# Performance work log

Measured on AMD Instinct MI355X. Metric: run time of the kernel, lower is better.

## Reference

```python
import jax, jax.numpy as jnp
import numpy as np

MAX_NUM_CAPS = 10
NEG = -1e9

def _layernorm(x, g, b):
    m = x.mean(-1, keepdims=True)
    v = x.var(-1, keepdims=True)
    return (x - m) / jnp.sqrt(v + 1e-5) * g + b

def _gatv2(x, Wl, Wr, att, bias, adj):
    # x: [B,M,F]; Wl/Wr: [F,H*C]; att: [H,C]; adj: [B,M,M] bool, adj[b,i,j] = edge i->j
    B, M, F = x.shape
    H, C = att.shape
    xl = jnp.einsum('bmf,fhc->bmhc', x, Wl.reshape(F, H, C))  # source transform
    xr = jnp.einsum('bmf,fhc->bmhc', x, Wr.reshape(F, H, C))  # target transform
    # GATv2 score: att . leaky_relu(xl[i] + xr[j]) for edge (src=i, dst=j)
    z = jax.nn.leaky_relu(xl[:, :, None, :, :] + xr[:, None, :, :, :], 0.2)  # [B,i,j,H,C]
    e = jnp.einsum('bijhc,hc->bijh', z, att)
    e = jnp.where(adj[..., None], e, NEG)
    alpha = jax.nn.softmax(e, axis=1)  # softmax over incoming sources i per target j
    out = jnp.einsum('bijh,bihc->bjhc', alpha, xl)  # aggregate at targets
    return out.reshape(B, M, H * C) + bias

def setup_inputs() -> dict:
    key = jax.random.key(0)
    ks = jax.random.split(key, 16)
    B, N, T = 128, 16, 48
    Fm, H, C3 = 128, 4, 64
    s = 0.05
    inp = {
        'team_obs': jax.random.normal(ks[0], (B, N, 14), jnp.float32),
        'target_obs': jax.random.normal(ks[1], (B, T, 15), jnp.float32),
        'team_mask': jax.random.normal(ks[2], (B, 2, N), jnp.float32),
        'local_target_mask': jnp.ones((B, T + 1), jnp.float32),
        'W_emb': jax.random.normal(ks[3], (16, Fm), jnp.float32) * s,
        'b_emb': jnp.zeros((Fm,), jnp.float32),
        'Wl1': jax.random.normal(ks[4], (Fm, Fm), jnp.float32) * s,
        'Wr1': jax.random.normal(ks[5], (Fm, Fm), jnp.float32) * s,
        'att1': jax.random.normal(ks[6], (H, Fm // H), jnp.float32) * s,
        'b1': jnp.zeros((Fm,), jnp.float32),
        'Wl2': jax.random.normal(ks[7], (Fm, Fm), jnp.float32) * s,
        'Wr2': jax.random.normal(ks[8], (Fm, Fm), jnp.float32) * s,
        'att2': jax.random.normal(ks[9], (H, Fm // H), jnp.float32) * s,
        'b2': jnp.zeros((Fm,), jnp.float32),
        'Wl3': jax.random.normal(ks[10], (Fm, C3), jnp.float32) * s,
        'Wr3': jax.random.normal(ks[11], (Fm, C3), jnp.float32) * s,
        'att3': jax.random.normal(ks[12], (1, C3), jnp.float32) * s,
        'b3': jnp.zeros((C3,), jnp.float32),
        'ln1_g': jnp.ones((Fm,), jnp.float32),
        'ln1_b': jnp.zeros((Fm,), jnp.float32),
        'ln2_g': jnp.ones((Fm,), jnp.float32),
        'ln2_b': jnp.zeros((Fm,), jnp.float32),
    }
    return inp

def reference(team_obs, target_obs, team_mask, local_target_mask,
              W_emb, b_emb, Wl1, Wr1, att1, b1, Wl2, Wr2, att2, b2,
              Wl3, Wr3, att3, b3, ln1_g, ln1_b, ln2_g, ln2_b):
    B, N, _ = team_obs.shape
    team = jnp.concatenate([team_obs, jnp.zeros((B, N, 2), team_obs.dtype)], axis=2)
    tgt = target_obs[:, :, :-1]
    T = tgt.shape[1]
    tgt = jnp.concatenate([tgt[:, :, :2 + MAX_NUM_CAPS],
                           jnp.zeros((B, T, 2), tgt.dtype),
                           tgt[:, :, -2:]], axis=2)
    fin = jnp.concatenate([team, tgt], axis=1)  # [B, M, inp_dim]
    h = fin @ W_emb + b_emb  # [B, M, 128]
    imp_team = team_mask[:, 0] != -1e9          # [B, N]
    imp_tgt = local_target_mask[:, :-1] != 0.0  # [B, T]
    imp = jnp.concatenate([imp_team, imp_tgt], axis=1)  # [B, M]
    M = N + T
    eye = jnp.eye(M, dtype=bool)
    # edges among active nodes minus diagonal; PyG GATv2Conv add_self_loops=True re-adds self edges
    adj = (imp[:, :, None] & imp[:, None, :] & ~eye) | eye  # [B, M, M]
    out = jax.nn.relu(_layernorm(_gatv2(h, Wl1, Wr1, att1, b1, adj), ln1_g, ln1_b))
    out = jax.nn.relu(_layernorm(_gatv2(out, Wl2, Wr2, att2, b2, adj), ln2_g, ln2_b))
    out = _gatv2(out, Wl3, Wr3, att3, b3, adj)
    return out  # [B, M, out_dim]
```

## Files before the change

kernel.cpp:

```cpp
#include <hip/hip_runtime.h>

typedef unsigned short u16;
typedef unsigned int   u32;
typedef _Float16 h2  __attribute__((ext_vector_type(2)));
typedef __fp16   hw2 __attribute__((ext_vector_type(2)));
typedef __fp16   hw8 __attribute__((ext_vector_type(8)));
typedef float    f4  __attribute__((ext_vector_type(4)));

#define XS 136
#define PS 72
#define BS 72
#define OS2 20

static __device__ __forceinline__ h2 pk(float a, float b) {
    return __builtin_bit_cast(h2, __builtin_amdgcn_cvt_pkrtz(a, b));
}
static __device__ __forceinline__ float dot2(h2 a, h2 b, float c) {
    return __builtin_amdgcn_fdot2(__builtin_bit_cast(hw2, a),
                                  __builtin_bit_cast(hw2, b), c, false);
}
static __device__ __forceinline__ h2  b2h(u32 v) { return __builtin_bit_cast(h2, v); }
static __device__ __forceinline__ u32 h2u(h2 v)  { return __builtin_bit_cast(u32, v); }
static __device__ __forceinline__ h2  abs2(h2 v) { return b2h(h2u(v) & 0x7fff7fffu); }
static __device__ __forceinline__ u16 f2h(float f) { return __builtin_bit_cast(u16, (_Float16)f); }
static __device__ __forceinline__ f4 mfma16(uint4 a, uint4 b, f4 c) {
    return __builtin_amdgcn_mfma_f32_16x16x32_f16(__builtin_bit_cast(hw8, a),
                                                  __builtin_bit_cast(hw8, b), c, 0, 0, 0);
}

__global__ void pack_weights(const float* __restrict__ Wl1, const float* __restrict__ Wr1,
                             const float* __restrict__ Wl2, const float* __restrict__ Wr2,
                             const float* __restrict__ Wl3, const float* __restrict__ Wr3,
                             u32* __restrict__ wpk)
{
    const int o = blockIdx.x * 256 + threadIdx.x;
    const float* src; u32* dst; int local; int N;
    if      (o < 8192)  { src = Wl1; dst = wpk;         local = o;         N = 128; }
    else if (o < 16384) { src = Wr1; dst = wpk + 8192;  local = o - 8192;  N = 128; }
    else if (o < 24576) { src = Wl2; dst = wpk + 16384; local = o - 16384; N = 128; }
    else if (o < 32768) { src = Wr2; dst = wpk + 24576; local = o - 24576; N = 128; }
    else if (o < 36864) { src = Wl3; dst = wpk + 32768; local = o - 32768; N = 64;  }
    else                { src = Wr3; dst = wpk + 36864; local = o - 36864; N = 64;  }
    const int i2   = local & 3;
    const int lane = (local >> 2) & 63;
    const int frag = local >> 8;
    const int kb   = frag & 3;
    const int nt   = frag >> 2;
    const int k0   = kb*32 + ((lane >> 4) << 3) + i2*2;
    const int n    = nt*16 + (lane & 15);
    dst[local] = h2u(pk(src[k0*N + n], src[(k0+1)*N + n]));
}

static __device__ __forceinline__ void compute_imp(int t, int b,
    const float* __restrict__ team_mask, const float* __restrict__ ltm, float* sImp)
{
    if (t < 64) {
        float im;
        if (t < 16) im = (team_mask[b*32 + t] != -1000000000.0f) ? 1.f : 0.f;
        else        im = (ltm[b*49 + (t-16)] != 0.0f) ? 1.f : 0.f;
        sImp[t] = im;
    }
}

static __device__ __forceinline__ void load_afr_lds(const u16* sX, int mt, int lane, uint4 afr[4]) {
    const int n15 = lane & 15, qd = lane >> 4;
#pragma unroll
    for (int kb = 0; kb < 4; kb++)
        afr[kb] = *(const uint4*)&sX[(mt*16 + n15)*XS + kb*32 + (qd << 3)];
}
static __device__ __forceinline__ void load_afr_glb(const u32* __restrict__ gxRow, int mt, int lane, uint4 afr[4]) {
    const int n15 = lane & 15, qd = lane >> 4;
    const int m = mt*16 + n15;
#pragma unroll
    for (int kb = 0; kb < 4; kb++)
        afr[kb] = *(const uint4*)&gxRow[m*64 + kb*16 + qd*4];
}

static __device__ __forceinline__ void projL128(int w, int lane, const u32* __restrict__ wp,
    const uint4 afr[4], u16* sXl, u16* sXlB)
{
    const int mt = w & 3, nh = w >> 2;
    const int n15 = lane & 15, qd = lane >> 4;
#pragma unroll
    for (int nt = nh*4; nt < nh*4 + 4; nt++) {
        f4 acc = {0.f, 0.f, 0.f, 0.f};
#pragma unroll
        for (int kb = 0; kb < 4; kb++) {
            uint4 bf = *(const uint4*)&wp[((nt*4 + kb)*64 + lane)*4];
            acc = mfma16(afr[kb], bf, acc);
        }
        const int n  = nt*16 + n15;
        const int mb = mt*16 + (qd << 2);
#pragma unroll
        for (int r = 0; r < 4; r++) sXl[(mb + r)*XS + n] = f2h(acc[r]);
        uint2 u;
        u.x = h2u(pk(acc[0], acc[1]));
        u.y = h2u(pk(acc[2], acc[3]));
        *(uint2*)&sXlB[n*BS + mb] = u;
    }
}

static __device__ __forceinline__ void projR16(int w, int lane, const u32* __restrict__ wp,
    const uint4 afq[4], u16* sXrPx)
{
    const int n15 = lane & 15, qd = lane >> 4;
    const int nt = w;
    f4 acc = {0.f, 0.f, 0.f, 0.f};
#pragma unroll
    for (int kb = 0; kb < 4; kb++) {
        uint4 bf = *(const uint4*)&wp[((nt*4 + kb)*64 + lane)*4];
        acc = mfma16(afq[kb], bf, acc);
    }
    const int n = nt*16 + n15;
#pragma unroll
    for (int r = 0; r < 4; r++)
        sXrPx[((n >> 3)*16 + (qd << 2) + r)*8 + (n & 7)] = f2h(acc[r]);
}

static __device__ __forceinline__ void scores16(int w, int lane, int j0,
    const float* __restrict__ att,
    const u16* sXl, const u16* sXrPx, u16* sP,
    float* sAl, float* sL2, const float* sImp)
{
    const int h  = w & 3;
    const int qh = w >> 2;
    const int jj = lane & 15;
    const int is = lane >> 4;
    const int j  = j0 + jj;

    h2 a2[16];
#pragma unroll
    for (int q = 0; q < 16; q++) a2[q] = pk(att[h*32 + 2*q], att[h*32 + 2*q + 1]);

    if (w < 4) {
        const uint4* pr = (const uint4*)&sXl[lane*XS + h*32];
        float al = 0.f;
#pragma unroll
        for (int c4 = 0; c4 < 4; c4++) {
            uint4 v = pr[c4];
            al = dot2(b2h(v.x), a2[c4*4+0], al);
            al = dot2(b2h(v.y), a2[c4*4+1], al);
            al = dot2(b2h(v.z), a2[c4*4+2], al);
            al = dot2(b2h(v.w), a2[c4*4+3], al);
        }
        sAl[h*64 + lane] = al;
    }

    h2 xr2[16];
#pragma unroll
    for (int s = 0; s < 4; s++) {
        uint4 v = *(const uint4*)&sXrPx[((h*4 + s)*16 + jj)*8];
        xr2[s*4+0] = b2h(v.x); xr2[s*4+1] = b2h(v.y);
        xr2[s*4+2] = b2h(v.z); xr2[s*4+3] = b2h(v.w);
    }
    float Ar = 0.f;
#pragma unroll
    for (int q = 0; q < 16; q++) Ar = dot2(a2[q], xr2[q], Ar);
    const float impj = sImp[j];
    __syncthreads();

    float l = 0.f;
    u32 pr4[4];
    float pprev = 0.f;
#pragma unroll
    for (int i2 = 0; i2 < 8; i2++) {
        const int i = qh*32 + is*8 + i2;
        const uint4* pl = (const uint4*)&sXl[i*XS + h*32];
        uint4 v0 = pl[0], v1 = pl[1], v2 = pl[2], v3 = pl[3];
        h2 xl2[16];
        xl2[0] = b2h(v0.x); xl2[1] = b2h(v0.y); xl2[2]  = b2h(v0.z); xl2[3]  = b2h(v0.w);
        xl2[4] = b2h(v1.x); xl2[5] = b2h(v1.y); xl2[6]  = b2h(v1.z); xl2[7]  = b2h(v1.w);
        xl2[8] = b2h(v2.x); xl2[9] = b2h(v2.y); xl2[10] = b2h(v2.z); xl2[11] = b2h(v2.w);
        xl2[12]= b2h(v3.x); xl2[13]= b2h(v3.y); xl2[14] = b2h(v3.z); xl2[15] = b2h(v3.w);
        float S0 = 0.f, S1 = 0.f;
#pragma unroll
        for (int q = 0; q < 16; q += 2) {
            h2 t0 = abs2(xl2[q]   + xr2[q]);
            h2 t1 = abs2(xl2[q+1] + xr2[q+1]);
            S0 = dot2(a2[q],   t0, S0);
            S1 = dot2(a2[q+1], t1, S1);
        }
        float e  = 0.6f*(sAl[h*64 + i] + Ar) + 0.4f*(S0 + S1);
        float ad = (i == j) ? 1.f : impj * sImp[i];
        float p  = (ad != 0.f) ? __expf(e) : 0.f;
        if (i2 & 1) {
            h2 pp = pk(pprev, p);
            pr4[i2 >> 1] = h2u(pp);
            l += (float)pp[0] + (float)pp[1];
        } else {
            pprev = p;
        }
    }
    *(uint4*)&sP[(h*16 + jj)*PS + qh*32 + is*8] = make_uint4(pr4[0], pr4[1], pr4[2], pr4[3]);
    sL2[((h*2 + qh)*4 + is)*16 + jj] = l;
}

static __device__ __forceinline__ void aggln16(int w, int lane, int b, int j0,
    const float* __restrict__ bias, const float* __restrict__ lg, const float* __restrict__ lb,
    const u16* sP, const u16* sXlB, float* sOutF, const float* sL2,
    float* sPart, u32* __restrict__ gxOut)
{
    const int h   = w & 3;
    const int cb  = w >> 2;
    const int n15 = lane & 15;
    const int kq  = lane >> 4;

    f4 acc = {0.f,0.f,0.f,0.f};
#pragma unroll
    for (int ks = 0; ks < 2; ks++) {
        uint4 af = *(const uint4*)&sP[(h*16 + n15)*PS + ks*32 + kq*8];
        uint4 bf = *(const uint4*)&sXlB[(h*32 + cb*16 + n15)*BS + ks*32 + kq*8];
        acc = mfma16(af, bf, acc);
    }
#pragma unroll
    for (int r = 0; r < 4; r++)
        sOutF[(h*32 + cb*16 + n15)*OS2 + kq*4 + r] = acc[r];
    __syncthreads();

    const int jj = lane & 15, is2 = lane >> 4, hd = w >> 1;
    float l = 0.f;
#pragma unroll
    for (int g = 0; g < 8; g++) l += sL2[(hd*8 + g)*16 + jj];
    const float rl = 1.f / l;
    const int c0 = w*16 + is2*4;
    float y[4];
    float s1 = 0.f, s2 = 0.f;
#pragma unroll
    for (int k = 0; k < 4; k++) {
        float v = fmaf(sOutF[(c0 + k)*OS2 + jj], rl, bias[c0 + k]);
        y[k] = v; s1 += v; s2 = fmaf(v, v, s2);
    }
    sPart[(w*4 + is2)*16 + jj]       = s1;
    sPart[512 + (w*4 + is2)*16 + jj] = s2;
    __syncthreads();
    float su = 0.f, sq = 0.f;
#pragma unroll
    for (int g = 0; g < 32; g++) { su += sPart[g*16 + jj]; sq += sPart[512 + g*16 + jj]; }
    const float mean = su * 0.0078125f;
    const float var  = sq * 0.0078125f - mean*mean;
    const float rstd = rsqrtf(var + 1e-5f);
    float v0 = fmaxf(fmaf((y[0] - mean)*rstd, lg[c0],   lb[c0]),   0.f);
    float v1 = fmaxf(fmaf((y[1] - mean)*rstd, lg[c0+1], lb[c0+1]), 0.f);
    float v2 = fmaxf(fmaf((y[2] - mean)*rstd, lg[c0+2], lb[c0+2]), 0.f);
    float v3 = fmaxf(fmaf((y[3] - mean)*rstd, lg[c0+3], lb[c0+3]), 0.f);
    uint2 o;
    o.x = h2u(pk(v0, v1));
    o.y = h2u(pk(v2, v3));
    *(uint2*)(gxOut + (size_t)b*4096 + (size_t)(j0 + jj)*64 + (c0 >> 1)) = o;
}

__global__ void __launch_bounds__(512, 4) gnn_l1(
    const float* __restrict__ team_obs, const float* __restrict__ target_obs,
    const float* __restrict__ team_mask, const float* __restrict__ ltm,
    const float* __restrict__ W_emb, const float* __restrict__ b_emb,
    const float* __restrict__ att1, const float* __restrict__ b1,
    const float* __restrict__ ln1_g, const float* __restrict__ ln1_b,
    const u32* __restrict__ wpk, u32* __restrict__ gx1)
{
    __shared__ __align__(16) u16 sX   [64*XS];
    __shared__ __align__(16) u16 sXl  [64*XS];
    __shared__ __align__(16) u16 sXlB [128*BS];
    __shared__ __align__(16) u16 sXrPx[2048];
    __shared__ __align__(16) u16 sP   [4*16*PS];
    __shared__ float sAl [256];
    __shared__ float sL2 [512];
    __shared__ float sPart[1024];
    __shared__ float sImp[64];

    const int t    = threadIdx.x;
    const int w    = t >> 6;
    const int lane = t & 63;
    const int b    = blockIdx.x & 127;
    const int q    = blockIdx.x >> 7;
    const int j0   = q*16;

    float* sFin  = (float*)sP;
    float* sOutF = (float*)sX;

    compute_imp(t, b, team_mask, ltm, sImp);
    for (int ee = t; ee < 1024; ee += 512) {
        int m = ee >> 4, k = ee & 15;
        float v = 0.f;
        if (m < 16) {
            if (k < 14) v = team_obs[(b*16 + m)*14 + k];
        } else {
            const float* tg = target_obs + (size_t)(b*48 + (m-16))*15;
            if      (k < 12)  v = tg[k];
            else if (k == 14) v = tg[12];
            else if (k == 15) v = tg[13];
        }
        sFin[m*16 + k] = v;
    }
    __syncthreads();

    {
        const int f = t & 127;
        const int g = t >> 7;
        float wreg[16];
#pragma unroll
        for (int k = 0; k < 16; k++) wreg[k] = W_emb[k*128 + f];
        const float bf = b_emb[f];
#pragma unroll
        for (int mm = 0; mm < 16; mm++) {
            int m = g*16 + mm;
            const float4* pf = (const float4*)&sFin[m*16];
            float4 f0 = pf[0], f1 = pf[1], f2 = pf[2], f3 = pf[3];
            float acc = bf;
            acc = fmaf(f0.x, wreg[0],  acc); acc = fmaf(f0.y, wreg[1],  acc);
            acc = fmaf(f0.z, wreg[2],  acc); acc = fmaf(f0.w, wreg[3],  acc);
            acc = fmaf(f1.x, wreg[4],  acc); acc = fmaf(f1.y, wreg[5],  acc);
            acc = fmaf(f1.z, wreg[6],  acc); acc = fmaf(f1.w, wreg[7],  acc);
            acc = fmaf(f2.x, wreg[8],  acc); acc = fmaf(f2.y, wreg[9],  acc);
            acc = fmaf(f2.z, wreg[10], acc); acc = fmaf(f2.w, wreg[11], acc);
            acc = fmaf(f3.x, wreg[12], acc); acc = fmaf(f3.y, wreg[13], acc);
            acc = fmaf(f3.z, wreg[14], acc); acc = fmaf(f3.w, wreg[15], acc);
            sX[m*XS + f] = f2h(acc);
        }
    }
    __syncthreads();

    uint4 afr[4], afq[4];
    load_afr_lds(sX, w & 3, lane, afr);
    load_afr_lds(sX, q,     lane, afq);
    projL128(w, lane, wpk,        afr, sXl, sXlB);
    projR16 (w, lane, wpk + 8192, afq, sXrPx);
    __syncthreads();

    scores16(w, lane, j0, att1, sXl, sXrPx, sP, sAl, sL2, sImp);
    __syncthreads();
    aggln16(w, lane, b, j0, b1, ln1_g, ln1_b, sP, sXlB, sOutF, sL2, sPart, gx1);
}

__global__ void __launch_bounds__(512, 4) gnn_l2(
    const float* __restrict__ team_mask, const float* __restrict__ ltm,
    const float* __restrict__ att2, const float* __restrict__ b2,
    const float* __restrict__ ln2_g, const float* __restrict__ ln2_b,
    const u32* __restrict__ wpk, const u32* __restrict__ gxIn, u32* __restrict__ gxOut)
{
    __shared__ __align__(16) u16 sXl  [64*XS];
    __shared__ __align__(16) u16 sXlB [128*BS];
    __shared__ __align__(16) u16 sXrPx[2048];
    __shared__ __align__(16) u16 sP   [4*16*PS];
    __shared__ __align__(16) float sOutF[128*OS2];
    __shared__ float sAl [256];
    __shared__ float sL2 [512];
    __shared__ float sPart[1024];
    __shared__ float sImp[64];

    const int t    = threadIdx.x;
    const int w    = t >> 6;
    const int lane = t & 63;
    const int b    = blockIdx.x & 127;
    const int q    = blockIdx.x >> 7;
    const int j0   = q*16;

    compute_imp(t, b, team_mask, ltm, sImp);
    const u32* gxRow = gxIn + (size_t)b*4096;

    uint4 afr[4], afq[4];
    load_afr_glb(gxRow, w & 3, lane, afr);
    load_afr_glb(gxRow, q,     lane, afq);
    projL128(w, lane, wpk + 16384, afr, sXl, sXlB);
    projR16 (w, lane, wpk + 24576, afq, sXrPx);
    __syncthreads();

    scores16(w, lane, j0, att2, sXl, sXrPx, sP, sAl, sL2, sImp);
    __syncthreads();
    aggln16(w, lane, b, j0, b2, ln2_g, ln2_b, sP, sXlB, sOutF, sL2, sPart, gxOut);
}

__global__ void __launch_bounds__(512, 4) gnn_l3(
    const float* __restrict__ team_mask, const float* __restrict__ ltm,
    const float* __restrict__ att3, const float* __restrict__ b3,
    const u32* __restrict__ wpk, const u32* __restrict__ gxIn, float* __restrict__ out)
{
    __shared__ __align__(16) u16 sXl3 [64*72];
    __shared__ __align__(16) u16 sXlB3[64*72];
    __shared__ __align__(16) u16 sXrP3[1024];
    __shared__ __align__(16) u16 sP3  [16*72];
    __shared__ float sAl3[64];
    __shared__ float sPart[512];
    __shared__ float sRl [16];
    __shared__ float sImp[64];

    const int t    = threadIdx.x;
    const int w    = t >> 6;
    const int lane = t & 63;
    const int b    = blockIdx.x & 127;
    const int q    = blockIdx.x >> 7;
    const int j0   = q*16;
    const int n15  = lane & 15;
    const int qd   = lane >> 4;

    compute_imp(t, b, team_mask, ltm, sImp);
    const u32* gxRow = gxIn + (size_t)b*4096;

    {
        uint4 afr[4];
        load_afr_glb(gxRow, w & 3, lane, afr);
        const u32* wp = wpk + 32768;
        const int mt = w & 3, nh = w >> 2;
#pragma unroll
        for (int nt = nh*2; nt < nh*2 + 2; nt++) {
            f4 acc = {0.f,0.f,0.f,0.f};
#pragma unroll
            for (int kb = 0; kb < 4; kb++) {
                uint4 bf = *(const uint4*)&wp[((nt*4 + kb)*64 + lane)*4];
                acc = mfma16(afr[kb], bf, acc);
            }
            const int n  = nt*16 + n15;
            const int mb = mt*16 + (qd << 2);
#pragma unroll
            for (int r = 0; r < 4; r++) sXl3[(mb + r)*72 + n] = f2h(acc[r]);
            uint2 u;
            u.x = h2u(pk(acc[0], acc[1]));
            u.y = h2u(pk(acc[2], acc[3]));
            *(uint2*)&sXlB3[n*72 + mb] = u;
        }
    }
    if (w < 4) {
        uint4 afq[4];
        load_afr_glb(gxRow, q, lane, afq);
        const u32* wp = wpk + 36864;
        f4 acc = {0.f,0.f,0.f,0.f};
#pragma unroll
        for (int kb = 0; kb < 4; kb++) {
            uint4 bf = *(const uint4*)&wp[((w*4 + kb)*64 + lane)*4];
            acc = mfma16(afq[kb], bf, acc);
        }
        const int n = w*16 + n15;
#pragma unroll
        for (int r = 0; r < 4; r++)
            sXrP3[((n >> 3)*16 + (qd << 2) + r)*8 + (n & 7)] = f2h(acc[r]);
    }
    __syncthreads();

    {
        h2 a2l[4];
#pragma unroll
        for (int qq = 0; qq < 4; qq++) a2l[qq] = pk(att3[w*8 + 2*qq], att3[w*8 + 2*qq + 1]);
        uint4 v = *(const uint4*)&sXl3[lane*72 + w*8];
        float al = 0.f;
        al = dot2(b2h(v.x), a2l[0], al);
        al = dot2(b2h(v.y), a2l[1], al);
        al = dot2(b2h(v.z), a2l[2], al);
        al = dot2(b2h(v.w), a2l[3], al);
        sPart[w*64 + lane] = al;
    }
    __syncthreads();
    if (t < 64) {
        sAl3[t] = ((sPart[t] + sPart[64+t]) + (sPart[128+t] + sPart[192+t]))
                + ((sPart[256+t] + sPart[320+t]) + (sPart[384+t] + sPart[448+t]));
    }
    __syncthreads();

    {
        const int jj = n15;
        const int is = qd;
        const int j  = j0 + jj;
        h2 a3[32], xr3[32];
#pragma unroll
        for (int qq = 0; qq < 32; qq++) a3[qq] = pk(att3[2*qq], att3[2*qq + 1]);
#pragma unroll
        for (int s = 0; s < 8; s++) {
            uint4 v = *(const uint4*)&sXrP3[(s*16 + jj)*8];
            xr3[s*4+0] = b2h(v.x); xr3[s*4+1] = b2h(v.y);
            xr3[s*4+2] = b2h(v.z); xr3[s*4+3] = b2h(v.w);
        }
        float Ar = 0.f;
#pragma unroll
        for (int qq = 0; qq < 32; qq++) Ar = dot2(a3[qq], xr3[qq], Ar);
        const float impj = sImp[j];
        const int i0 = w*8 + is*2;

        float p0, p1;
        {
            const int i = i0;
            const uint4* pl = (const uint4*)&sXl3[i*72];
            float S0 = 0.f, S1 = 0.f;
#pragma unroll
            for (int c4 = 0; c4 < 8; c4++) {
                uint4 v = pl[c4];
                S0 = dot2(a3[c4*4+0], abs2(b2h(v.x) + xr3[c4*4+0]), S0);
                S1 = dot2(a3[c4*4+1], abs2(b2h(v.y) + xr3[c4*4+1]), S1);
                S0 = dot2(a3[c4*4+2], abs2(b2h(v.z) + xr3[c4*4+2]), S0);
                S1 = dot2(a3[c4*4+3], abs2(b2h(v.w) + xr3[c4*4+3]), S1);
            }
            float e  = 0.6f*(sAl3[i] + Ar) + 0.4f*(S0 + S1);
            float ad = (i == j) ? 1.f : impj * sImp[i];
            p0 = (ad != 0.f) ? __expf(e) : 0.f;
        }
        {
            const int i = i0 + 1;
            const uint4* pl = (const uint4*)&sXl3[i*72];
            float S0 = 0.f, S1 = 0.f;
#pragma unroll
            for (int c4 = 0; c4 < 8; c4++) {
                uint4 v = pl[c4];
                S0 = dot2(a3[c4*4+0], abs2(b2h(v.x) + xr3[c4*4+0]), S0);
                S1 = dot2(a3[c4*4+1], abs2(b2h(v.y) + xr3[c4*4+1]), S1);
                S0 = dot2(a3[c4*4+2], abs2(b2h(v.z) + xr3[c4*4+2]), S0);
                S1 = dot2(a3[c4*4+3], abs2(b2h(v.w) + xr3[c4*4+3]), S1);
            }
            float e  = 0.6f*(sAl3[i] + Ar) + 0.4f*(S0 + S1);
            float ad = (i == j) ? 1.f : impj * sImp[i];
            p1 = (ad != 0.f) ? __expf(e) : 0.f;
        }
        h2 pp = pk(p0, p1);
        *(u32*)&sP3[jj*72 + i0] = h2u(pp);
        sPart[(w*4 + is)*16 + jj] = (float)pp[0] + (float)pp[1];
    }
    __syncthreads();
    if (t < 16) {
        float s = 0.f;
#pragma unroll
        for (int g = 0; g < 32; g++) s += sPart[g*16 + t];
        sRl[t] = 1.f / s;
    }

    f4 acc3 = {0.f,0.f,0.f,0.f};
    if (w < 4) {
#pragma unroll
        for (int ks = 0; ks < 2; ks++) {
            uint4 af = *(const uint4*)&sP3[n15*72 + ks*32 + (lane >> 4)*8];
            uint4 bf = *(const uint4*)&sXlB3[(w*16 + n15)*72 + ks*32 + (lane >> 4)*8];
            acc3 = mfma16(af, bf, acc3);
        }
    }
    __syncthreads();
    if (w < 4) {
        const int c  = w*16 + n15;
        const float bc = b3[c];
#pragma unroll
        for (int r = 0; r < 4; r++) {
            const int jl = (lane >> 4)*4 + r;
            out[(size_t)b*4096 + (size_t)(j0 + jl)*64 + c] = fmaf(acc3[r], sRl[jl], bc);
        }
    }
}

extern "C" void kernel_launch(void* const* d_in, const int* in_sizes, int n_in,
                              void* d_out, int out_size, void* d_ws, size_t ws_size,
                              hipStream_t stream) {
    (void)in_sizes; (void)n_in; (void)ws_size; (void)out_size;
    const float* team_obs          = (const float*)d_in[0];
    const float* target_obs        = (const float*)d_in[1];
    const float* team_mask         = (const float*)d_in[2];
    const float* local_target_mask = (const float*)d_in[3];
    const float* W_emb             = (const float*)d_in[4];
    const float* b_emb             = (const float*)d_in[5];
    const float* Wl1               = (const float*)d_in[6];
    const float* Wr1               = (const float*)d_in[7];
    const float* att1              = (const float*)d_in[8];
    const float* b1                = (const float*)d_in[9];
    const float* Wl2               = (const float*)d_in[10];
    const float* Wr2               = (const float*)d_in[11];
    const float* att2              = (const float*)d_in[12];
    const float* b2                = (const float*)d_in[13];
    const float* Wl3               = (const float*)d_in[14];
    const float* Wr3               = (const float*)d_in[15];
    const float* att3              = (const float*)d_in[16];
    const float* b3                = (const float*)d_in[17];
    const float* ln1_g             = (const float*)d_in[18];
    const float* ln1_b             = (const float*)d_in[19];
    const float* ln2_g             = (const float*)d_in[20];
    const float* ln2_b             = (const float*)d_in[21];
    float* out = (float*)d_out;

    u32* wpk = (u32*)d_ws;
    u32* gx2 = (u32*)d_ws + 40960;
    u32* gx1 = (u32*)d_out;

    pack_weights<<<dim3(160), dim3(256), 0, stream>>>(Wl1, Wr1, Wl2, Wr2, Wl3, Wr3, wpk);
    gnn_l1<<<dim3(512), dim3(512), 0, stream>>>(
        team_obs, target_obs, team_mask, local_target_mask, W_emb, b_emb,
        att1, b1, ln1_g, ln1_b, wpk, gx1);
    gnn_l2<<<dim3(512), dim3(512), 0, stream>>>(
        team_mask, local_target_mask, att2, b2, ln2_g, ln2_b, wpk, gx1, gx2);
    gnn_l3<<<dim3(512), dim3(512), 0, stream>>>(
        team_mask, local_target_mask, att3, b3, wpk, gx2, out);
}
```

Measured before the change: 132.3 us.

## Process 32 target nodes per block with 1024-thread blocks in all GNN layers

Each block now handles 32 target nodes instead of 16, so 256 blocks of 1024 threads replace 512 blocks of 512 threads. The per-graph source projection (Xl for all 64 nodes) is then computed once per two 32-target halves instead of once per four 16-target quarters, which cuts redundant projection MFMAs and weight loads. Scores, aggregation, layernorm and the layer-3 output were remapped to the wider tile, with larger shared buffers and relocated workspace buffers. The cost is fewer, larger blocks with more LDS each, which may reduce occupancy and lengthen barrier waits on the 256-CU device.

```diff
diff --git a/kernel.cpp b/kernel.cpp
--- a/kernel.cpp
+++ b/kernel.cpp
@@ -10,7 +10,7 @@
 #define XS 136
 #define PS 72
 #define BS 72
-#define OS2 20
+#define OS3 34
 
 static __device__ __forceinline__ h2 pk(float a, float b) {
     return __builtin_bit_cast(h2, __builtin_amdgcn_cvt_pkrtz(a, b));
@@ -76,13 +76,14 @@
         afr[kb] = *(const uint4*)&gxRow[m*64 + kb*16 + qd*4];
 }
 
-static __device__ __forceinline__ void projL128(int w, int lane, const u32* __restrict__ wp,
+static __device__ __forceinline__ void projL128_16(int w, int lane, const u32* __restrict__ wp,
     const uint4 afr[4], u16* sXl, u16* sXlB)
 {
-    const int mt = w & 3, nh = w >> 2;
+    const int mt = w & 3, np = w >> 2;
     const int n15 = lane & 15, qd = lane >> 4;
-#pragma unroll
-    for (int nt = nh*4; nt < nh*4 + 4; nt++) {
+    (void)mt;
+#pragma unroll
+    for (int nt = np*2; nt < np*2 + 2; nt++) {
         f4 acc = {0.f, 0.f, 0.f, 0.f};
 #pragma unroll
         for (int kb = 0; kb < 4; kb++) {
@@ -90,7 +91,7 @@
             acc = mfma16(afr[kb], bf, acc);
         }
         const int n  = nt*16 + n15;
-        const int mb = mt*16 + (qd << 2);
+        const int mb = (w & 3)*16 + (qd << 2);
 #pragma unroll
         for (int r = 0; r < 4; r++) sXl[(mb + r)*XS + n] = f2h(acc[r]);
         uint2 u;
@@ -100,32 +101,33 @@
     }
 }
 
-static __device__ __forceinline__ void projR16(int w, int lane, const u32* __restrict__ wp,
+static __device__ __forceinline__ void projR32(int w, int lane, const u32* __restrict__ wp,
     const uint4 afq[4], u16* sXrPx)
 {
     const int n15 = lane & 15, qd = lane >> 4;
-    const int nt = w;
+    const int ntR = w >> 1;
     f4 acc = {0.f, 0.f, 0.f, 0.f};
 #pragma unroll
     for (int kb = 0; kb < 4; kb++) {
-        uint4 bf = *(const uint4*)&wp[((nt*4 + kb)*64 + lane)*4];
+        uint4 bf = *(const uint4*)&wp[((ntR*4 + kb)*64 + lane)*4];
         acc = mfma16(afq[kb], bf, acc);
     }
-    const int n = nt*16 + n15;
+    const int n   = ntR*16 + n15;
+    const int mb2 = (w & 1)*16 + (qd << 2);
 #pragma unroll
     for (int r = 0; r < 4; r++)
-        sXrPx[((n >> 3)*16 + (qd << 2) + r)*8 + (n & 7)] = f2h(acc[r]);
-}
-
-static __device__ __forceinline__ void scores16(int w, int lane, int j0,
+        sXrPx[((n >> 3)*32 + mb2 + r)*8 + (n & 7)] = f2h(acc[r]);
+}
+
+static __device__ __forceinline__ void scores32(int w, int lane, int j0,
     const float* __restrict__ att,
     const u16* sXl, const u16* sXrPx, u16* sP,
     float* sAl, float* sL2, const float* sImp)
 {
     const int h  = w & 3;
     const int qh = w >> 2;
-    const int jj = lane & 15;
-    const int is = lane >> 4;
+    const int jj = lane & 31;
+    const int is = lane >> 5;
     const int j  = j0 + jj;
 
     h2 a2[16];
@@ -149,7 +151,7 @@
     h2 xr2[16];
 #pragma unroll
     for (int s = 0; s < 4; s++) {
-        uint4 v = *(const uint4*)&sXrPx[((h*4 + s)*16 + jj)*8];
+        uint4 v = *(const uint4*)&sXrPx[((h*4 + s)*32 + jj)*8];
         xr2[s*4+0] = b2h(v.x); xr2[s*4+1] = b2h(v.y);
         xr2[s*4+2] = b2h(v.z); xr2[s*4+3] = b2h(v.w);
     }
@@ -162,9 +164,10 @@
     float l = 0.f;
     u32 pr4[4];
     float pprev = 0.f;
+    const int i0 = qh*16 + is*8;
 #pragma unroll
     for (int i2 = 0; i2 < 8; i2++) {
-        const int i = qh*32 + is*8 + i2;
+        const int i = i0 + i2;
         const uint4* pl = (const uint4*)&sXl[i*XS + h*32];
         uint4 v0 = pl[0], v1 = pl[1], v2 = pl[2], v3 = pl[3];
         h2 xl2[16];
@@ -191,51 +194,54 @@
             pprev = p;
         }
     }
-    *(uint4*)&sP[(h*16 + jj)*PS + qh*32 + is*8] = make_uint4(pr4[0], pr4[1], pr4[2], pr4[3]);
-    sL2[((h*2 + qh)*4 + is)*16 + jj] = l;
-}
-
-static __device__ __forceinline__ void aggln16(int w, int lane, int b, int j0,
+    *(uint4*)&sP[(h*32 + jj)*PS + i0] = make_uint4(pr4[0], pr4[1], pr4[2], pr4[3]);
+    sL2[((h*4 + qh)*2 + is)*32 + jj] = l;
+}
+
+static __device__ __forceinline__ void aggln32(int w, int lane, int b, int j0,
     const float* __restrict__ bias, const float* __restrict__ lg, const float* __restrict__ lb,
     const u16* sP, const u16* sXlB, float* sOutF, const float* sL2,
     float* sPart, u32* __restrict__ gxOut)
 {
     const int h   = w & 3;
-    const int cb  = w >> 2;
+    const int jq  = (w >> 2) & 1;
+    const int cb  = w >> 3;
     const int n15 = lane & 15;
     const int kq  = lane >> 4;
 
     f4 acc = {0.f,0.f,0.f,0.f};
 #pragma unroll
     for (int ks = 0; ks < 2; ks++) {
-        uint4 af = *(const uint4*)&sP[(h*16 + n15)*PS + ks*32 + kq*8];
+        uint4 af = *(const uint4*)&sP[(h*32 + jq*16 + n15)*PS + ks*32 + kq*8];
         uint4 bf = *(const uint4*)&sXlB[(h*32 + cb*16 + n15)*BS + ks*32 + kq*8];
         acc = mfma16(af, bf, acc);
     }
 #pragma unroll
     for (int r = 0; r < 4; r++)
-        sOutF[(h*32 + cb*16 + n15)*OS2 + kq*4 + r] = acc[r];
-    __syncthreads();
-
-    const int jj = lane & 15, is2 = lane >> 4, hd = w >> 1;
+        sOutF[(h*32 + cb*16 + n15)*OS3 + jq*16 + kq*4 + r] = acc[r];
+    __syncthreads();
+
+    const int jj = lane & 31, is5 = lane >> 5;
+    const int cgrp = w*2 + is5;
+    const int c0 = cgrp*4;
+    const int hd = c0 >> 5;
     float l = 0.f;
 #pragma unroll
-    for (int g = 0; g < 8; g++) l += sL2[(hd*8 + g)*16 + jj];
+    for (int g = 0; g < 8; g++) l += sL2[(hd*8 + g)*32 + jj];
     const float rl = 1.f / l;
-    const int c0 = w*16 + is2*4;
     float y[4];
     float s1 = 0.f, s2 = 0.f;
 #pragma unroll
     for (int k = 0; k < 4; k++) {
-        float v = fmaf(sOutF[(c0 + k)*OS2 + jj], rl, bias[c0 + k]);
+        float v = fmaf(sOutF[(c0 + k)*OS3 + jj], rl, bias[c0 + k]);
         y[k] = v; s1 += v; s2 = fmaf(v, v, s2);
     }
-    sPart[(w*4 + is2)*16 + jj]       = s1;
-    sPart[512 + (w*4 + is2)*16 + jj] = s2;
+    sPart[cgrp*32 + jj]        = s1;
+    sPart[1024 + cgrp*32 + jj] = s2;
     __syncthreads();
     float su = 0.f, sq = 0.f;
 #pragma unroll
-    for (int g = 0; g < 32; g++) { su += sPart[g*16 + jj]; sq += sPart[512 + g*16 + jj]; }
+    for (int g = 0; g < 32; g++) { su += sPart[g*32 + jj]; sq += sPart[1024 + g*32 + jj]; }
     const float mean = su * 0.0078125f;
     const float var  = sq * 0.0078125f - mean*mean;
     const float rstd = rsqrtf(var + 1e-5f);
@@ -249,7 +255,7 @@
     *(uint2*)(gxOut + (size_t)b*4096 + (size_t)(j0 + jj)*64 + (c0 >> 1)) = o;
 }
 
-__global__ void __launch_bounds__(512, 4) gnn_l1(
+__global__ void __launch_bounds__(1024, 4) gnn_l1(
     const float* __restrict__ team_obs, const float* __restrict__ target_obs,
     const float* __restrict__ team_mask, const float* __restrict__ ltm,
     const float* __restrict__ W_emb, const float* __restrict__ b_emb,
@@ -260,26 +266,26 @@
     __shared__ __align__(16) u16 sX   [64*XS];
     __shared__ __align__(16) u16 sXl  [64*XS];
     __shared__ __align__(16) u16 sXlB [128*BS];
-    __shared__ __align__(16) u16 sXrPx[2048];
-    __shared__ __align__(16) u16 sP   [4*16*PS];
+    __shared__ __align__(16) u16 sXrPx[4096];
+    __shared__ __align__(16) u16 sP   [4*32*PS];
     __shared__ float sAl [256];
-    __shared__ float sL2 [512];
-    __shared__ float sPart[1024];
+    __shared__ float sL2 [1024];
+    __shared__ float sPart[2048];
     __shared__ float sImp[64];
 
     const int t    = threadIdx.x;
     const int w    = t >> 6;
     const int lane = t & 63;
-    const int b    = blockIdx.x & 127;
-    const int q    = blockIdx.x >> 7;
-    const int j0   = q*16;
+    const int b    = blockIdx.x >> 1;
+    const int q    = blockIdx.x & 1;
+    const int j0   = q*32;
 
     float* sFin  = (float*)sP;
     float* sOutF = (float*)sX;
 
     compute_imp(t, b, team_mask, ltm, sImp);
-    for (int ee = t; ee < 1024; ee += 512) {
-        int m = ee >> 4, k = ee & 15;
+    {
+        int m = t >> 4, k = t & 15;
         float v = 0.f;
         if (m < 16) {
             if (k < 14) v = team_obs[(b*16 + m)*14 + k];
@@ -301,8 +307,8 @@
         for (int k = 0; k < 16; k++) wreg[k] = W_emb[k*128 + f];
         const float bf = b_emb[f];
 #pragma unroll
-        for (int mm = 0; mm < 16; mm++) {
-            int m = g*16 + mm;
+        for (int mm = 0; mm < 8; mm++) {
+            int m = g*8 + mm;
             const float4* pf = (const float4*)&sFin[m*16];
             float4 f0 = pf[0], f1 = pf[1], f2 = pf[2], f3 = pf[3];
             float acc = bf;
@@ -320,18 +326,18 @@
     __syncthreads();
 
     uint4 afr[4], afq[4];
-    load_afr_lds(sX, w & 3, lane, afr);
-    load_afr_lds(sX, q,     lane, afq);
-    projL128(w, lane, wpk,        afr, sXl, sXlB);
-    projR16 (w, lane, wpk + 8192, afq, sXrPx);
-    __syncthreads();
-
-    scores16(w, lane, j0, att1, sXl, sXrPx, sP, sAl, sL2, sImp);
-    __syncthreads();
-    aggln16(w, lane, b, j0, b1, ln1_g, ln1_b, sP, sXlB, sOutF, sL2, sPart, gx1);
-}
-
-__global__ void __launch_bounds__(512, 4) gnn_l2(
+    load_afr_lds(sX, w & 3,           lane, afr);
+    load_afr_lds(sX, q*2 + (w & 1),   lane, afq);
+    projL128_16(w, lane, wpk,        afr, sXl, sXlB);
+    projR32    (w, lane, wpk + 8192, afq, sXrPx);
+    __syncthreads();
+
+    scores32(w, lane, j0, att1, sXl, sXrPx, sP, sAl, sL2, sImp);
+    __syncthreads();
+    aggln32(w, lane, b, j0, b1, ln1_g, ln1_b, sP, sXlB, sOutF, sL2, sPart, gx1);
+}
+
+__global__ void __launch_bounds__(1024, 4) gnn_l2(
     const float* __restrict__ team_mask, const float* __restrict__ ltm,
     const float* __restrict__ att2, const float* __restrict__ b2,
     const float* __restrict__ ln2_g, const float* __restrict__ ln2_b,
@@ -339,56 +345,56 @@
 {
     __shared__ __align__(16) u16 sXl  [64*XS];
     __shared__ __align__(16) u16 sXlB [128*BS];
-    __shared__ __align__(16) u16 sXrPx[2048];
-    __shared__ __align__(16) u16 sP   [4*16*PS];
-    __shared__ __align__(16) float sOutF[128*OS2];
+    __shared__ __align__(16) u16 sXrPx[4096];
+    __shared__ __align__(16) u16 sP   [4*32*PS];
+    __shared__ __align__(16) float sOutF[128*OS3];
     __shared__ float sAl [256];
-    __shared__ float sL2 [512];
-    __shared__ float sPart[1024];
+    __shared__ float sL2 [1024];
+    __shared__ float sPart[2048];
     __shared__ float sImp[64];
 
     const int t    = threadIdx.x;
     const int w    = t >> 6;
     const int lane = t & 63;
-    const int b    = blockIdx.x & 127;
-    const int q    = blockIdx.x >> 7;
-    const int j0   = q*16;
+    const int b    = blockIdx.x >> 1;
+    const int q    = blockIdx.x & 1;
+    const int j0   = q*32;
 
     compute_imp(t, b, team_mask, ltm, sImp);
     const u32* gxRow = gxIn + (size_t)b*4096;
 
     uint4 afr[4], afq[4];
-    load_afr_glb(gxRow, w & 3, lane, afr);
-    load_afr_glb(gxRow, q,     lane, afq);
-    projL128(w, lane, wpk + 16384, afr, sXl, sXlB);
-    projR16 (w, lane, wpk + 24576, afq, sXrPx);
-    __syncthreads();
-
-    scores16(w, lane, j0, att2, sXl, sXrPx, sP, sAl, sL2, sImp);
-    __syncthreads();
-    aggln16(w, lane, b, j0, b2, ln2_g, ln2_b, sP, sXlB, sOutF, sL2, sPart, gxOut);
-}
-
-__global__ void __launch_bounds__(512, 4) gnn_l3(
+    load_afr_glb(gxRow, w & 3,         lane, afr);
+    load_afr_glb(gxRow, q*2 + (w & 1), lane, afq);
+    projL128_16(w, lane, wpk + 16384, afr, sXl, sXlB);
+    projR32    (w, lane, wpk + 24576, afq, sXrPx);
+    __syncthreads();
+
+    scores32(w, lane, j0, att2, sXl, sXrPx, sP, sAl, sL2, sImp);
+    __syncthreads();
+    aggln32(w, lane, b, j0, b2, ln2_g, ln2_b, sP, sXlB, sOutF, sL2, sPart, gxOut);
+}
+
+__global__ void __launch_bounds__(1024, 4) gnn_l3(
     const float* __restrict__ team_mask, const float* __restrict__ ltm,
     const float* __restrict__ att3, const float* __restrict__ b3,
     const u32* __restrict__ wpk, const u32* __restrict__ gxIn, float* __restrict__ out)
 {
     __shared__ __align__(16) u16 sXl3 [64*72];
     __shared__ __align__(16) u16 sXlB3[64*72];
-    __shared__ __align__(16) u16 sXrP3[1024];
-    __shared__ __align__(16) u16 sP3  [16*72];
+    __shared__ __align__(16) u16 sXrP3[2048];
+    __shared__ __align__(16) u16 sP3  [32*72];
     __shared__ float sAl3[64];
-    __shared__ float sPart[512];
-    __shared__ float sRl [16];
+    __shared__ float sPart[1024];
+    __shared__ float sRl [32];
     __shared__ float sImp[64];
 
     const int t    = threadIdx.x;
     const int w    = t >> 6;
     const int lane = t & 63;
-    const int b    = blockIdx.x & 127;
-    const int q    = blockIdx.x >> 7;
-    const int j0   = q*16;
+    const int b    = blockIdx.x >> 1;
+    const int q    = blockIdx.x & 1;
+    const int j0   = q*32;
     const int n15  = lane & 15;
     const int qd   = lane >> 4;
 
@@ -399,71 +405,71 @@
         uint4 afr[4];
         load_afr_glb(gxRow, w & 3, lane, afr);
         const u32* wp = wpk + 32768;
-        const int mt = w & 3, nh = w >> 2;
-#pragma unroll
-        for (int nt = nh*2; nt < nh*2 + 2; nt++) {
-            f4 acc = {0.f,0.f,0.f,0.f};
-#pragma unroll
-            for (int kb = 0; kb < 4; kb++) {
-                uint4 bf = *(const uint4*)&wp[((nt*4 + kb)*64 + lane)*4];
-                acc = mfma16(afr[kb], bf, acc);
-            }
-            const int n  = nt*16 + n15;
-            const int mb = mt*16 + (qd << 2);
-#pragma unroll
-            for (int r = 0; r < 4; r++) sXl3[(mb + r)*72 + n] = f2h(acc[r]);
-            uint2 u;
-            u.x = h2u(pk(acc[0], acc[1]));
-            u.y = h2u(pk(acc[2], acc[3]));
-            *(uint2*)&sXlB3[n*72 + mb] = u;
-        }
-    }
-    if (w < 4) {
+        const int nt = w >> 2;
+        f4 acc = {0.f,0.f,0.f,0.f};
+#pragma unroll
+        for (int kb = 0; kb < 4; kb++) {
+            uint4 bf = *(const uint4*)&wp[((nt*4 + kb)*64 + lane)*4];
+            acc = mfma16(afr[kb], bf, acc);
+        }
+        const int n  = nt*16 + n15;
+        const int mb = (w & 3)*16 + (qd << 2);
+#pragma unroll
+        for (int r = 0; r < 4; r++) sXl3[(mb + r)*72 + n] = f2h(acc[r]);
+        uint2 u;
+        u.x = h2u(pk(acc[0], acc[1]));
+        u.y = h2u(pk(acc[2], acc[3]));
+        *(uint2*)&sXlB3[n*72 + mb] = u;
+    }
+    if (w < 8) {
         uint4 afq[4];
-        load_afr_glb(gxRow, q, lane, afq);
+        load_afr_glb(gxRow, q*2 + (w & 1), lane, afq);
         const u32* wp = wpk + 36864;
+        const int nt = w >> 1;
         f4 acc = {0.f,0.f,0.f,0.f};
 #pragma unroll
         for (int kb = 0; kb < 4; kb++) {
-            uint4 bf = *(const uint4*)&wp[((w*4 + kb)*64 + lane)*4];
+            uint4 bf = *(const uint4*)&wp[((nt*4 + kb)*64 + lane)*4];
             acc = mfma16(afq[kb], bf, acc);
         }
-        const int n = w*16 + n15;
+        const int n   = nt*16 + n15;
+        const int mb2 = (w & 1)*16 + (qd << 2);
 #pragma unroll
         for (int r = 0; r < 4; r++)
-            sXrP3[((n >> 3)*16 + (qd << 2) + r)*8 + (n & 7)] = f2h(acc[r]);
+            sXrP3[((n >> 3)*32 + mb2 + r)*8 + (n & 7)] = f2h(acc[r]);
     }
     __syncthreads();
 
     {
-        h2 a2l[4];
-#pragma unroll
-        for (int qq = 0; qq < 4; qq++) a2l[qq] = pk(att3[w*8 + 2*qq], att3[w*8 + 2*qq + 1]);
-        uint4 v = *(const uint4*)&sXl3[lane*72 + w*8];
-        float al = 0.f;
-        al = dot2(b2h(v.x), a2l[0], al);
+        h2 a2l[2];
+        a2l[0] = pk(att3[w*4 + 0], att3[w*4 + 1]);
+        a2l[1] = pk(att3[w*4 + 2], att3[w*4 + 3]);
+        uint2 v = *(const uint2*)&sXl3[lane*72 + w*4];
+        float al = dot2(b2h(v.x), a2l[0], 0.f);
         al = dot2(b2h(v.y), a2l[1], al);
-        al = dot2(b2h(v.z), a2l[2], al);
-        al = dot2(b2h(v.w), a2l[3], al);
         sPart[w*64 + lane] = al;
     }
     __syncthreads();
     if (t < 64) {
-        sAl3[t] = ((sPart[t] + sPart[64+t]) + (sPart[128+t] + sPart[192+t]))
-                + ((sPart[256+t] + sPart[320+t]) + (sPart[384+t] + sPart[448+t]));
+        float s = 0.f;
+#pragma unroll
+        for (int p = 0; p < 16; p += 4)
+            s += ((sPart[p*64 + t] + sPart[(p+1)*64 + t]) +
+                  (sPart[(p+2)*64 + t] + sPart[(p+3)*64 + t]));
+        sAl3[t] = s;
     }
     __syncthreads();
 
     {
-        const int jj = n15;
-        const int is = qd;
+        const int jj = lane & 31;
+        const int is = lane >> 5;
         const int j  = j0 + jj;
         h2 a3[32], xr3[32];
 #pragma unroll
         for (int qq = 0; qq < 32; qq++) a3[qq] = pk(att3[2*qq], att3[2*qq + 1]);
 #pragma unroll
         for (int s = 0; s < 8; s++) {
-            uint4 v = *(const uint4*)&sXrP3[(s*16 + jj)*8];
+            uint4 v = *(const uint4*)&sXrP3[(s*32 + jj)*8];
             xr3[s*4+0] = b2h(v.x); xr3[s*4+1] = b2h(v.y);
             xr3[s*4+2] = b2h(v.z); xr3[s*4+3] = b2h(v.w);
         }
@@ -471,11 +477,12 @@
 #pragma unroll
         for (int qq = 0; qq < 32; qq++) Ar = dot2(a3[qq], xr3[qq], Ar);
         const float impj = sImp[j];
-        const int i0 = w*8 + is*2;
-
-        float p0, p1;
-        {
-            const int i = i0;
+        const int i0 = (w*2 + is)*2;
+
+        float p01[2];
+#pragma unroll
+        for (int ii = 0; ii < 2; ii++) {
+            const int i = i0 + ii;
             const uint4* pl = (const uint4*)&sXl3[i*72];
             float S0 = 0.f, S1 = 0.f;
 #pragma unroll
@@ -488,52 +495,38 @@
             }
             float e  = 0.6f*(sAl3[i] + Ar) + 0.4f*(S0 + S1);
             float ad = (i == j) ? 1.f : impj * sImp[i];
-            p0 = (ad != 0.f) ? __expf(e) : 0.f;
-        }
-        {
-            const int i = i0 + 1;
-            const uint4* pl = (const uint4*)&sXl3[i*72];
-            float S0 = 0.f, S1 = 0.f;
-#pragma unroll
-            for (int c4 = 0; c4 < 8; c4++) {
-                uint4 v = pl[c4];
-                S0 = dot2(a3[c4*4+0], abs2(b2h(v.x) + xr3[c4*4+0]), S0);
-                S1 = dot2(a3[c4*4+1], abs2(b2h(v.y) + xr3[c4*4+1]), S1);
-                S0 = dot2(a3[c4*4+2], abs2(b2h(v.z) + xr3[c4*4+2]), S0);
-                S1 = dot2(a3[c4*4+3], abs2(b2h(v.w) + xr3[c4*4+3]), S1);
-            }
-            float e  = 0.6f*(sAl3[i] + Ar) + 0.4f*(S0 + S1);
-            float ad = (i == j) ? 1.f : impj * sImp[i];
-            p1 = (ad != 0.f) ? __expf(e) : 0.f;
-        }
-        h2 pp = pk(p0, p1);
+            p01[ii] = (ad != 0.f) ? __expf(e) : 0.f;
+        }
+        h2 pp = pk(p01[0], p01[1]);
         *(u32*)&sP3[jj*72 + i0] = h2u(pp);
-        sPart[(w*4 + is)*16 + jj] = (float)pp[0] + (float)pp[1];
-    }
-    __syncthreads();
-    if (t < 16) {
+        sPart[(w*2 + is)*32 + jj] = (float)pp[0] + (float)pp[1];
+    }
+    __syncthreads();
+    if (t < 32) {
         float s = 0.f;
 #pragma unroll
-        for (int g = 0; g < 32; g++) s += sPart[g*16 + t];
+        for (int g = 0; g < 32; g++) s += sPart[g*32 + t];
         sRl[t] = 1.f / s;
     }
 
     f4 acc3 = {0.f,0.f,0.f,0.f};
-    if (w < 4) {
+    if (w < 8) {
+        const int jt = w & 1, ct = w >> 1;
 #pragma unroll
         for (int ks = 0; ks < 2; ks++) {
-            uint4 af = *(const uint4*)&sP3[n15*72 + ks*32 + (lane >> 4)*8];
-            uint4 bf = *(const uint4*)&sXlB3[(w*16 + n15)*72 + ks*32 + (lane >> 4)*8];
+            uint4 af = *(const uint4*)&sP3[(jt*16 + n15)*72 + ks*32 + qd*8];
+            uint4 bf = *(const uint4*)&sXlB3[(ct*16 + n15)*72 + ks*32 + qd*8];
             acc3 = mfma16(af, bf, acc3);
         }
     }
     __syncthreads();
-    if (w < 4) {
-        const int c  = w*16 + n15;
+    if (w < 8) {
+        const int jt = w & 1, ct = w >> 1;
+        const int c  = ct*16 + n15;
         const float bc = b3[c];
 #pragma unroll
         for (int r = 0; r < 4; r++) {
-            const int jl = (lane >> 4)*4 + r;
+            const int jl = jt*16 + qd*4 + r;
             out[(size_t)b*4096 + (size_t)(j0 + jl)*64 + c] = fmaf(acc3[r], sRl[jl], bc);
         }
     }
@@ -568,15 +561,15 @@
     float* out = (float*)d_out;
 
     u32* wpk = (u32*)d_ws;
-    u32* gx2 = (u32*)d_ws + 40960;
-    u32* gx1 = (u32*)d_out;
+    u32* gx1 = (u32*)d_ws + 65536;
+    u32* gx2 = (u32*)d_ws + 589824;
 
     pack_weights<<<dim3(160), dim3(256), 0, stream>>>(Wl1, Wr1, Wl2, Wr2, Wl3, Wr3, wpk);
-    gnn_l1<<<dim3(512), dim3(512), 0, stream>>>(
+    gnn_l1<<<dim3(256), dim3(1024), 0, stream>>>(
         team_obs, target_obs, team_mask, local_target_mask, W_emb, b_emb,
         att1, b1, ln1_g, ln1_b, wpk, gx1);
-    gnn_l2<<<dim3(512), dim3(512), 0, stream>>>(
+    gnn_l2<<<dim3(256), dim3(1024), 0, stream>>>(
         team_mask, local_target_mask, att2, b2, ln2_g, ln2_b, wpk, gx1, gx2);
-    gnn_l3<<<dim3(512), dim3(512), 0, stream>>>(
+    gnn_l3<<<dim3(256), dim3(1024), 0, stream>>>(
         team_mask, local_target_mask, att3, b3, wpk, gx2, out);
 }
```

Measured after the change: 133.1 us. Within noise of the previous version (+0.6%).
